# Kernel optimization log

Measured on AMD Instinct MI355X. Metric: run time of the kernel, lower is better.

## Reference

```python
import jax, jax.numpy as jnp
import numpy as np

N, E, R = 10000, 320000, 32
IN, H, OUT, REL_IN = 256, 256, 256, 768
GAMMA = 10.0


def _seg_softmax(logits, seg, n):
    # numerically stable softmax over edges grouped by target node
    m = jax.ops.segment_max(logits, seg, num_segments=n)
    e = jnp.exp(logits - m[seg])
    s = jax.ops.segment_sum(e, seg, num_segments=n)
    return e / (s[seg] + 1e-16)


def _rgat_layer(x, src, dst, etype, W, q, k, n):
    # per-relation linear transform of all nodes: [N, R, H]
    xt = jnp.einsum('ni,rio->nro', x, W)
    xj = xt[src, etype]          # [E, H] transformed source feats
    xi = xt[dst, etype]          # [E, H] transformed target feats
    logits = jax.nn.leaky_relu((xi * q[etype]).sum(-1) + (xj * k[etype]).sum(-1), 0.2)
    a = _seg_softmax(logits, dst, n)            # [E]
    return jax.ops.segment_sum(a[:, None] * xj, dst, num_segments=n)  # [N, H]


def setup_inputs() -> dict:
    key = jax.random.key(0)
    ks = jax.random.split(key, 16)
    s = 0.05
    return {
        'x': jax.random.normal(ks[0], (N, IN), jnp.float32),
        'edge_index': jax.random.randint(ks[1], (2, E), 0, N, jnp.int32),
        'edge_type': jax.random.randint(ks[2], (E,), 0, R, jnp.int32),
        'W1': jax.random.normal(ks[3], (R, IN, H), jnp.float32) * s,
        'q1': jax.random.normal(ks[4], (R, H), jnp.float32) * s,
        'k1': jax.random.normal(ks[5], (R, H), jnp.float32) * s,
        'W2': jax.random.normal(ks[6], (R, H, H), jnp.float32) * s,
        'q2': jax.random.normal(ks[7], (R, H), jnp.float32) * s,
        'k2': jax.random.normal(ks[8], (R, H), jnp.float32) * s,
        'lin_w': jax.random.normal(ks[9], (H, OUT), jnp.float32) * s,
        'lin_b': jnp.zeros((OUT,), jnp.float32),
        'rel_bert': jax.random.normal(ks[10], (R, REL_IN), jnp.float32),
        'rel_lin_w': jax.random.normal(ks[11], (REL_IN, H), jnp.float32) * s,
        'rel_lin_b': jnp.zeros((H,), jnp.float32),
    }


def reference(x, edge_index, edge_type, W1, q1, k1, W2, q2, k2,
              lin_w, lin_b, rel_bert, rel_lin_w, rel_lin_b):
    src, dst = edge_index[0], edge_index[1]
    h = jax.nn.relu(_rgat_layer(x, src, dst, edge_type, W1, q1, k1, N))
    h = jax.nn.relu(_rgat_layer(h, src, dst, edge_type, W2, q2, k2, N))
    h = h @ lin_w + lin_b                                   # [N, OUT]
    # relation embeddings (dropout omitted: eval-mode determinism)
    rel = jax.nn.relu(rel_bert @ rel_lin_w + rel_lin_b)     # [R, H]
    # TransE scoring per edge
    diff = h[src] + rel[edge_type] - h[dst]                 # [E, OUT]
    score = GAMMA - jnp.abs(diff).sum(-1)                   # [E]
    return score
```

## Files before the change

kernel.cpp:

```cpp
#include <hip/hip_runtime.h>
#include <hip/hip_bf16.h>
#include <stdint.h>

#define R_ 32
#define H_ 256
#define GAMMA_ 10.0f

typedef __attribute__((ext_vector_type(4))) float f32x4;
typedef __attribute__((ext_vector_type(8))) short bf16x8;

__device__ __forceinline__ unsigned short f2b(float f){
  union { float f; unsigned u; } v; v.f = f;
  unsigned r = v.u + 0x7FFFu + ((v.u >> 16) & 1u);
  return (unsigned short)(r >> 16);
}
__device__ __forceinline__ float b2f(unsigned short h){
  union { unsigned u; float f; } v; v.u = ((unsigned)h) << 16; return v.f;
}

__global__ __launch_bounds__(256) void prep_kernel(
    const float* __restrict__ x, unsigned short* __restrict__ xb, int n4,
    const float* __restrict__ W1, unsigned short* __restrict__ Wt1,
    const float* __restrict__ W2, unsigned short* __restrict__ Wt2,
    const float* __restrict__ lin_w, unsigned short* __restrict__ linT,
    const float* __restrict__ q1, const float* __restrict__ k1, float* __restrict__ wqkT1,
    const float* __restrict__ q2, const float* __restrict__ k2, float* __restrict__ wqkT2,
    const float* __restrict__ rb, const float* __restrict__ rw,
    const float* __restrict__ rbias, unsigned short* __restrict__ relb,
    const int* __restrict__ dst, const int* __restrict__ et, int* __restrict__ cnt2, int E,
    int nb0, int nb_tw, int nb_lin, int nb_wqk, int nb_rel, int nb_hist){
  __shared__ float tile[32][33];
  const int bx = blockIdx.x, t = threadIdx.x;
  const int b0 = nb0, b1 = b0 + nb_tw, b2 = b1 + nb_tw, b3 = b2 + nb_lin;
  const int b4 = b3 + nb_wqk, b5 = b4 + nb_wqk, b6 = b5 + nb_rel;

  if (bx < b0){
    int i = bx * 256 + t;
    if (i < n4){
      float4 v = ((const float4*)x)[i];
      ushort4 o; o.x=f2b(v.x); o.y=f2b(v.y); o.z=f2b(v.z); o.w=f2b(v.w);
      ((ushort4*)xb)[i] = o;
    }
    return;
  }
  if (bx < b3){
    const float* W; unsigned short* Wt; int local;
    if (bx < b1){ W = W1; Wt = Wt1; local = bx - b0; }
    else if (bx < b2){ W = W2; Wt = Wt2; local = bx - b1; }
    else { W = lin_w; Wt = linT; local = bx - b2; }
    int i0 = (local & 7) * 32, o0 = ((local >> 3) & 7) * 32, r = local >> 6;
    int tx = t & 31, ty = t >> 5;
    const float* Wr = W + (size_t)r * 65536;
    for (int rr = ty; rr < 32; rr += 8)
      tile[rr][tx] = Wr[(size_t)(i0 + rr) * 256 + o0 + tx];
    __syncthreads();
    unsigned short* outr = Wt + (size_t)r * 65536;
    for (int rr = ty; rr < 32; rr += 8)
      outr[(size_t)(o0 + rr) * 256 + i0 + tx] = f2b(tile[tx][rr]);
    return;
  }
  if (bx < b5){
    bool first = bx < b4;
    int local = bx - (first ? b3 : b4);
    int w = t >> 6, lane = t & 63;
    int p = local * 4 + w;
    int i = p & 255, r = p >> 8;
    const float* W  = first ? W1 : W2;
    const float* qv = first ? q1 : q2;
    const float* kv = first ? k1 : k2;
    const float* row = W + ((size_t)r * 256 + i) * 256;
    float sq = 0.f, sk = 0.f;
    #pragma unroll
    for (int q4 = 0; q4 < 4; ++q4){
      int o = lane + q4 * 64;
      float wv = row[o];
      sq += wv * qv[r * 256 + o];
      sk += wv * kv[r * 256 + o];
    }
    #pragma unroll
    for (int o = 32; o; o >>= 1){ sq += __shfl_xor(sq, o); sk += __shfl_xor(sk, o); }
    if (!lane){
      float* wq = first ? wqkT1 : wqkT2;
      wq[i * 64 + r] = sq; wq[i * 64 + 32 + r] = sk;
    }
    return;
  }
  if (bx < b6){
    int r = bx - b5, h = t;
    float acc = rbias[h];
    const float* br = rb + (size_t)r * 768;
    for (int i = 0; i < 768; ++i) acc += br[i] * rw[(size_t)i * 256 + h];
    relb[r * 256 + h] = f2b(fmaxf(acc, 0.f));
    return;
  }
  {
    int e = (bx - b6) * 256 + t;
    if (e < E){
      int d = dst[e];
      atomicAdd(&cnt2[(d >> 5) * 1024 + (d & 31) * 32 + et[e]], 1);
    }
  }
}

__global__ void totred_kernel(const int* __restrict__ cnt2, int* __restrict__ tot){
  __shared__ int red[256];
  int blk = blockIdx.x, t = threadIdx.x;
  int s = 0;
  #pragma unroll
  for (int q = 0; q < 4; ++q) s += cnt2[blk * 1024 + q * 256 + t];
  red[t] = s; __syncthreads();
  for (int o = 128; o; o >>= 1){ if (t < o) red[t] += red[t + o]; __syncthreads(); }
  if (!t) tot[blk] = red[0];
}
__global__ void scan_kernel(const int* __restrict__ deg, int* __restrict__ off, int n){
  __shared__ int carry;
  __shared__ int buf[1024];
  if (threadIdx.x == 0) carry = 0;
  __syncthreads();
  for (int base = 0; base < n; base += 1024){
    int i = base + threadIdx.x;
    int v = (i < n) ? deg[i] : 0;
    buf[threadIdx.x] = v; __syncthreads();
    for (int o = 1; o < 1024; o <<= 1){
      int t = (threadIdx.x >= o) ? buf[threadIdx.x - o] : 0;
      __syncthreads();
      buf[threadIdx.x] += t;
      __syncthreads();
    }
    if (i < n) off[i] = carry + buf[threadIdx.x] - v;
    __syncthreads();
    if (threadIdx.x == 1023) carry += buf[1023];
    __syncthreads();
  }
  if (threadIdx.x == 0) off[n] = carry;
}
__global__ __launch_bounds__(256) void ps2scan_kernel(const int* __restrict__ cnt2, const int* __restrict__ base,
                                                      int* __restrict__ ps2, int nblk, int nbins){
  __shared__ int sb[1024];
  int blk = blockIdx.x, t = threadIdx.x;
  int orig[4];
  #pragma unroll
  for (int q = 0; q < 4; ++q){ int i = q * 256 + t; orig[q] = cnt2[blk * 1024 + i]; sb[i] = orig[q]; }
  __syncthreads();
  for (int o = 1; o < 1024; o <<= 1){
    int v[4];
    #pragma unroll
    for (int q = 0; q < 4; ++q){ int i = q * 256 + t; v[q] = (i >= o) ? sb[i - o] : 0; }
    __syncthreads();
    #pragma unroll
    for (int q = 0; q < 4; ++q){ int i = q * 256 + t; sb[i] += v[q]; }
    __syncthreads();
  }
  int b = base[blk];
  #pragma unroll
  for (int q = 0; q < 4; ++q){ int i = q * 256 + t; ps2[blk * 1024 + i] = b + sb[i] - orig[q]; }
  if (blk == 0 && t == 0) ps2[nbins] = base[nblk];
}
__global__ void scatter2_kernel(const int* __restrict__ src, const int* __restrict__ dst,
                                const int* __restrict__ et, const int* __restrict__ ps2,
                                int* __restrict__ cur2, int* __restrict__ es_src,
                                int* __restrict__ es_et, int E){
  int e = blockIdx.x * 256 + threadIdx.x;
  if (e >= E) return;
  int d = dst[e], r = et[e];
  int key = (d >> 5) * 1024 + (d & 31) * 32 + r;
  int pos = ps2[key] + atomicAdd(&cur2[key], 1);
  es_src[pos] = src[e];
  es_et[pos]  = r;
}

template<int MODE>
__global__ __launch_bounds__(256) void gemmq_kernel(
    const unsigned short* __restrict__ A, const unsigned short* __restrict__ Bt,
    unsigned short* __restrict__ C, const float* __restrict__ bias, int M, int g_gemm,
    const float* __restrict__ wqkT, float* __restrict__ qdot, float* __restrict__ kdot){
  __shared__ unsigned short As[2][128 * 64];
  __shared__ unsigned short Bs[2][128 * 64];
  const int tid = threadIdx.x, lane = tid & 63, wid = tid >> 6;
  const int bx = blockIdx.x;

  if (MODE == 0 && bx >= g_gemm){
    int node = (bx - g_gemm) * 4 + wid;
    if (node >= M) return;
    float* xr = ((float*)As) + wid * 256;
    ushort4 v = ((const ushort4*)(A + (size_t)node * 256))[lane];
    xr[lane * 4 + 0] = b2f(v.x);
    xr[lane * 4 + 1] = b2f(v.y);
    xr[lane * 4 + 2] = b2f(v.z);
    xr[lane * 4 + 3] = b2f(v.w);
    float acc = 0.f;
    #pragma unroll 8
    for (int kk = 0; kk < 256; ++kk)
      acc = fmaf(xr[kk], wqkT[kk * 64 + lane], acc);
    if (lane < 32) qdot[node * 32 + lane] = acc;
    else           kdot[node * 32 + lane - 32] = acc;
    return;
  }

  const int x = (MODE == 0) ? (bx & 63) : (bx & 1);
  const int y = (MODE == 0) ? (bx >> 6) : (bx >> 1);
  const int r = (MODE == 0) ? (x >> 1) : 0;
  const int nbase = (x & 1) * 128;
  const int mbase = y * 128;
  const int wm = (wid >> 1) * 64, wn = (wid & 1) * 64;
  const int lg = lane >> 4, lr = lane & 15;
  const unsigned short* Brel = Bt + (size_t)r * 65536;

  f32x4 acc[4][4];
  #pragma unroll
  for (int i = 0; i < 4; ++i)
    #pragma unroll
    for (int j = 0; j < 4; ++j) acc[i][j] = (f32x4)0.0f;

  auto stage = [&](int buf, int kt){
    #pragma unroll
    for (int q = 0; q < 4; ++q){
      int ci  = (q * 4 + wid) * 64 + lane;
      int row = ci >> 3, p = ci & 7;
      int gch = p ^ (row & 7);
      int grow = mbase + row; if (grow >= M) grow = M - 1;
      const unsigned short* ga = A + (size_t)grow * 256 + kt * 64 + gch * 8;
      __builtin_amdgcn_global_load_lds((const __attribute__((address_space(1))) void*)ga,
          (__attribute__((address_space(3))) void*)(As[buf] + (size_t)(q * 4 + wid) * 512), 16, 0, 0);
      const unsigned short* gb = Brel + (size_t)(nbase + row) * 256 + kt * 64 + gch * 8;
      __builtin_amdgcn_global_load_lds((const __attribute__((address_space(1))) void*)gb,
          (__attribute__((address_space(3))) void*)(Bs[buf] + (size_t)(q * 4 + wid) * 512), 16, 0, 0);
    }
  };

  stage(0, 0);
  __syncthreads();

  for (int kt = 0; kt < 4; ++kt){
    const int cur = kt & 1;
    if (kt < 3) stage(cur ^ 1, kt + 1);
    #pragma unroll
    for (int kk = 0; kk < 2; ++kk){
      bf16x8 af[4], bg[4];
      #pragma unroll
      for (int mi = 0; mi < 4; ++mi){
        int row = wm + mi * 16 + lr;
        int pc = (lg + kk * 4) ^ (row & 7);
        af[mi] = *(const bf16x8*)&As[cur][row * 64 + pc * 8];
      }
      #pragma unroll
      for (int ni = 0; ni < 4; ++ni){
        int row = wn + ni * 16 + lr;
        int pc = (lg + kk * 4) ^ (row & 7);
        bg[ni] = *(const bf16x8*)&Bs[cur][row * 64 + pc * 8];
      }
      #pragma unroll
      for (int mi = 0; mi < 4; ++mi)
        #pragma unroll
        for (int ni = 0; ni < 4; ++ni)
          acc[mi][ni] = __builtin_amdgcn_mfma_f32_16x16x32_bf16(af[mi], bg[ni], acc[mi][ni], 0, 0, 0);
    }
    __syncthreads();
  }

  unsigned short* c_lds = (unsigned short*)As;
  #pragma unroll
  for (int mi = 0; mi < 4; ++mi){
    #pragma unroll
    for (int j = 0; j < 4; ++j){
      int row = wm + mi * 16 + lg * 4 + j;
      #pragma unroll
      for (int ni = 0; ni < 4; ++ni){
        int col = wn + ni * 16 + lr;
        float v = acc[mi][ni][j];
        if (MODE == 1) v += bias[nbase + col];
        c_lds[row * 136 + col] = f2b(v);
      }
    }
  }
  __syncthreads();
  #pragma unroll
  for (int it = 0; it < 8; ++it){
    int c = it * 256 + tid;
    int row = c >> 4, ch = c & 15;
    int rowm = mbase + row;
    if (rowm < M){
      bf16x8 v = *(const bf16x8*)&c_lds[row * 136 + ch * 8];
      if (MODE == 0) *(bf16x8*)&C[((size_t)r * M + rowm) * H_ + nbase + ch * 8] = v;
      else           *(bf16x8*)&C[(size_t)rowm * H_ + nbase + ch * 8] = v;
    }
  }
}

__global__ void attn_agg_kernel(const unsigned short* __restrict__ xt, const float* __restrict__ qdot,
                                const float* __restrict__ kdot, const int* __restrict__ ps2,
                                const int* __restrict__ es_src, const int* __restrict__ es_et,
                                float* __restrict__ a, unsigned short* __restrict__ hout, int n){
  int w = threadIdx.x >> 6, lane = threadIdx.x & 63;
  int node = blockIdx.x * 4 + w;
  if (node >= n) return;
  int kb = (node >> 5) * 1024 + (node & 31) * 32;
  int s = 0, e = 0;
  float qd = 0.f;
  if (lane < 32){
    s = ps2[kb + lane]; e = ps2[kb + lane + 1];
    qd = qdot[node * 32 + lane];
  }
  float m = -1e30f;
  for (int j = s; j < e; ++j){
    float z = qd + kdot[es_src[j] * 32 + lane];
    z = (z > 0.f) ? z : 0.2f * z;
    a[j] = z;
    m = fmaxf(m, z);
  }
  #pragma unroll
  for (int o = 32; o; o >>= 1) m = fmaxf(m, __shfl_xor(m, o));
  float sum = 0.f;
  for (int j = s; j < e; ++j){
    float ez = __expf(a[j] - m);
    a[j] = ez; sum += ez;
  }
  #pragma unroll
  for (int o = 32; o; o >>= 1) sum += __shfl_xor(sum, o);
  float inv = 1.0f / (sum + 1e-16f);
  int s0 = ps2[kb], s1 = ps2[kb + 32];
  float a0 = 0.f, a1 = 0.f, a2 = 0.f, a3 = 0.f;
  int j = s0;
  for (; j + 4 <= s1; j += 4){
    int sc0 = es_src[j],   et0 = es_et[j];
    int sc1 = es_src[j+1], et1 = es_et[j+1];
    int sc2 = es_src[j+2], et2 = es_et[j+2];
    int sc3 = es_src[j+3], et3 = es_et[j+3];
    float w0 = a[j], w1 = a[j+1], w2 = a[j+2], w3 = a[j+3];
    ushort4 v0 = ((const ushort4*)(xt + ((size_t)et0 * n + sc0) * 256))[lane];
    ushort4 v1 = ((const ushort4*)(xt + ((size_t)et1 * n + sc1) * 256))[lane];
    ushort4 v2 = ((const ushort4*)(xt + ((size_t)et2 * n + sc2) * 256))[lane];
    ushort4 v3 = ((const ushort4*)(xt + ((size_t)et3 * n + sc3) * 256))[lane];
    a0 += w0*b2f(v0.x) + w1*b2f(v1.x) + w2*b2f(v2.x) + w3*b2f(v3.x);
    a1 += w0*b2f(v0.y) + w1*b2f(v1.y) + w2*b2f(v2.y) + w3*b2f(v3.y);
    a2 += w0*b2f(v0.z) + w1*b2f(v1.z) + w2*b2f(v2.z) + w3*b2f(v3.z);
    a3 += w0*b2f(v0.w) + w1*b2f(v1.w) + w2*b2f(v2.w) + w3*b2f(v3.w);
  }
  for (; j < s1; ++j){
    int sc = es_src[j], et = es_et[j];
    float wv = a[j];
    ushort4 v = ((const ushort4*)(xt + ((size_t)et * n + sc) * 256))[lane];
    a0 = fmaf(wv, b2f(v.x), a0);
    a1 = fmaf(wv, b2f(v.y), a1);
    a2 = fmaf(wv, b2f(v.z), a2);
    a3 = fmaf(wv, b2f(v.w), a3);
  }
  ushort4 o;
  o.x = f2b(fmaxf(a0 * inv, 0.f)); o.y = f2b(fmaxf(a1 * inv, 0.f));
  o.z = f2b(fmaxf(a2 * inv, 0.f)); o.w = f2b(fmaxf(a3 * inv, 0.f));
  ((ushort4*)(hout + (size_t)node * H_))[lane] = o;
}

__global__ void score_kernel(const unsigned short* __restrict__ hb, const unsigned short* __restrict__ relb,
                             const int* __restrict__ src_a, const int* __restrict__ dst_a,
                             const int* __restrict__ et_a, float* __restrict__ out, int E){
  int e = blockIdx.x * 4 + (threadIdx.x >> 6);
  int lane = threadIdx.x & 63;
  if (e >= E) return;
  int s = src_a[e], d = dst_a[e], r = et_a[e];
  ushort4 a4 = ((const ushort4*)(hb + (size_t)s * H_))[lane];
  ushort4 b4 = ((const ushort4*)(hb + (size_t)d * H_))[lane];
  ushort4 r4 = ((const ushort4*)(relb + (size_t)r * H_))[lane];
  float sum = fabsf(b2f(a4.x) + b2f(r4.x) - b2f(b4.x))
            + fabsf(b2f(a4.y) + b2f(r4.y) - b2f(b4.y))
            + fabsf(b2f(a4.z) + b2f(r4.z) - b2f(b4.z))
            + fabsf(b2f(a4.w) + b2f(r4.w) - b2f(b4.w));
  #pragma unroll
  for (int o = 32; o; o >>= 1) sum += __shfl_xor(sum, o);
  if (!lane) out[e] = GAMMA_ - sum;
}

extern "C" void kernel_launch(void* const* d_in, const int* in_sizes, int n_in,
                              void* d_out, int out_size, void* d_ws, size_t ws_size,
                              hipStream_t stream){
  const float* x         = (const float*)d_in[0];
  const int*   edge_idx  = (const int*)d_in[1];
  const int*   edge_type = (const int*)d_in[2];
  const float* W1        = (const float*)d_in[3];
  const float* q1        = (const float*)d_in[4];
  const float* k1        = (const float*)d_in[5];
  const float* W2        = (const float*)d_in[6];
  const float* q2        = (const float*)d_in[7];
  const float* k2        = (const float*)d_in[8];
  const float* lin_w     = (const float*)d_in[9];
  const float* lin_b     = (const float*)d_in[10];
  const float* rel_bert  = (const float*)d_in[11];
  const float* rel_lin_w = (const float*)d_in[12];
  const float* rel_lin_b = (const float*)d_in[13];
  float* score = (float*)d_out;

  const int Nn = in_sizes[0] / H_;
  const int E  = in_sizes[1] / 2;
  const int* src_a = edge_idx;
  const int* dst_a = edge_idx + E;
  const int NBLK  = (Nn + 31) / 32;
  const int NBINS = NBLK * 1024;

  char* ws = (char*)d_ws;
  size_t cur_off = 0;
  auto carve = [&](size_t bytes)->char*{
    char* p = ws + cur_off;
    cur_off += (bytes + 255) & ~(size_t)255;
    return p;
  };
  unsigned short* xt   = (unsigned short*)carve((size_t)Nn * R_ * H_ * 2);
  unsigned short* xb   = (unsigned short*)carve((size_t)Nn * H_ * 2);
  unsigned short* h1   = (unsigned short*)carve((size_t)Nn * H_ * 2);
  unsigned short* h2   = (unsigned short*)carve((size_t)Nn * H_ * 2);
  unsigned short* outb = (unsigned short*)carve((size_t)Nn * H_ * 2);
  unsigned short* Wt1  = (unsigned short*)carve((size_t)R_ * 65536 * 2);
  unsigned short* Wt2  = (unsigned short*)carve((size_t)R_ * 65536 * 2);
  unsigned short* linT = (unsigned short*)carve(65536 * 2);
  unsigned short* relb = (unsigned short*)carve(R_ * H_ * 2);
  float* wqkT1 = (float*)carve(64 * H_ * 4);
  float* wqkT2 = (float*)carve(64 * H_ * 4);
  float* qdot  = (float*)carve((size_t)Nn * R_ * 4);
  float* kdot  = (float*)carve((size_t)Nn * R_ * 4);
  int* cnt2    = (int*)carve((size_t)NBINS * 4);
  int* cur2    = (int*)carve((size_t)NBINS * 4);
  int* tot     = (int*)carve((size_t)NBLK * 4);
  int* baseA   = (int*)carve((size_t)(NBLK + 1) * 4);
  int* ps2     = (int*)carve((size_t)(NBINS + 1) * 4);
  int* es_src  = (int*)carve((size_t)E * 4);
  int* es_et   = (int*)carve((size_t)E * 4);
  float* attn  = (float*)carve((size_t)E * 4);
  (void)ws_size; (void)n_in; (void)out_size;

  const int mt = (Nn + 127) / 128;
  const int g_gemm = 64 * mt;
  const int nqd = (Nn + 3) / 4;

  const int n4 = Nn * H_ / 4;
  const int nb0 = (n4 + 255) / 256, nb_tw = 2048, nb_lin = 64, nb_wqk = 2048, nb_rel = 32;
  const int nb_hist = (E + 255) / 256;
  const int nprep = nb0 + 2 * nb_tw + nb_lin + 2 * nb_wqk + nb_rel + nb_hist;

  hipMemsetAsync(cnt2, 0, (size_t)NBINS * 4, stream);
  hipMemsetAsync(cur2, 0, (size_t)NBINS * 4, stream);

  prep_kernel<<<nprep, 256, 0, stream>>>(
      x, xb, n4, W1, Wt1, W2, Wt2, lin_w, linT,
      q1, k1, wqkT1, q2, k2, wqkT2,
      rel_bert, rel_lin_w, rel_lin_b, relb,
      dst_a, edge_type, cnt2, E,
      nb0, nb_tw, nb_lin, nb_wqk, nb_rel, nb_hist);

  totred_kernel<<<NBLK, 256, 0, stream>>>(cnt2, tot);
  scan_kernel<<<1, 1024, 0, stream>>>(tot, baseA, NBLK);
  ps2scan_kernel<<<NBLK, 256, 0, stream>>>(cnt2, baseA, ps2, NBLK, NBINS);
  scatter2_kernel<<<(E + 255) / 256, 256, 0, stream>>>(src_a, dst_a, edge_type, ps2, cur2, es_src, es_et, E);

  gemmq_kernel<0><<<g_gemm + nqd, 256, 0, stream>>>(xb, Wt1, xt, nullptr, Nn, g_gemm, wqkT1, qdot, kdot);
  attn_agg_kernel<<<nqd, 256, 0, stream>>>(xt, qdot, kdot, ps2, es_src, es_et, attn, h1, Nn);

  gemmq_kernel<0><<<g_gemm + nqd, 256, 0, stream>>>(h1, Wt2, xt, nullptr, Nn, g_gemm, wqkT2, qdot, kdot);
  attn_agg_kernel<<<nqd, 256, 0, stream>>>(xt, qdot, kdot, ps2, es_src, es_et, attn, h2, Nn);

  gemmq_kernel<1><<<2 * mt, 256, 0, stream>>>(h2, linT, outb, lin_b, Nn, 2 * mt, nullptr, nullptr, nullptr);
  score_kernel<<<(E + 3) / 4, 256, 0, stream>>>(outb, relb, src_a, dst_a, edge_type, score, E);
}
```

Before: 397.8 us.

## Split qdot projection into its own kernel and store GEMM output directly

```diff
diff --git a/kernel.cpp b/kernel.cpp
--- a/kernel.cpp
+++ b/kernel.cpp
@@ -169,39 +169,38 @@
   es_et[pos]  = r;
 }
 
+__global__ void qdot_kernel(const unsigned short* __restrict__ xb, const float* __restrict__ wqkT,
+                            float* __restrict__ qdot, float* __restrict__ kdot, int n){
+  __shared__ float xrow[4][256];
+  int w = threadIdx.x >> 6, lane = threadIdx.x & 63;
+  int node = blockIdx.x * 4 + w;
+  if (node >= n) return;
+  ushort4 v = ((const ushort4*)(xb + (size_t)node * 256))[lane];
+  float* xr = xrow[w];
+  xr[lane * 4 + 0] = b2f(v.x);
+  xr[lane * 4 + 1] = b2f(v.y);
+  xr[lane * 4 + 2] = b2f(v.z);
+  xr[lane * 4 + 3] = b2f(v.w);
+  float acc = 0.f;
+  #pragma unroll 8
+  for (int kk = 0; kk < 256; ++kk)
+    acc = fmaf(xr[kk], wqkT[kk * 64 + lane], acc);
+  if (lane < 32) qdot[node * 32 + lane] = acc;
+  else           kdot[node * 32 + lane - 32] = acc;
+}
+
 template<int MODE>
 __global__ __launch_bounds__(256) void gemmq_kernel(
     const unsigned short* __restrict__ A, const unsigned short* __restrict__ Bt,
-    unsigned short* __restrict__ C, const float* __restrict__ bias, int M, int g_gemm,
-    const float* __restrict__ wqkT, float* __restrict__ qdot, float* __restrict__ kdot){
+    unsigned short* __restrict__ C, const float* __restrict__ bias, int M, int NB){
   __shared__ unsigned short As[2][128 * 64];
   __shared__ unsigned short Bs[2][128 * 64];
-  const int tid = threadIdx.x, lane = tid & 63, wid = tid >> 6;
-  const int bx = blockIdx.x;
-
-  if (MODE == 0 && bx >= g_gemm){
-    int node = (bx - g_gemm) * 4 + wid;
-    if (node >= M) return;
-    float* xr = ((float*)As) + wid * 256;
-    ushort4 v = ((const ushort4*)(A + (size_t)node * 256))[lane];
-    xr[lane * 4 + 0] = b2f(v.x);
-    xr[lane * 4 + 1] = b2f(v.y);
-    xr[lane * 4 + 2] = b2f(v.z);
-    xr[lane * 4 + 3] = b2f(v.w);
-    float acc = 0.f;
-    #pragma unroll 8
-    for (int kk = 0; kk < 256; ++kk)
-      acc = fmaf(xr[kk], wqkT[kk * 64 + lane], acc);
-    if (lane < 32) qdot[node * 32 + lane] = acc;
-    else           kdot[node * 32 + lane - 32] = acc;
-    return;
-  }
-
-  const int x = (MODE == 0) ? (bx & 63) : (bx & 1);
-  const int y = (MODE == 0) ? (bx >> 6) : (bx >> 1);
-  const int r = (MODE == 0) ? (x >> 1) : 0;
-  const int nbase = (x & 1) * 128;
-  const int mbase = y * 128;
+  const int r     = blockIdx.x / NB;
+  const int nbase = (blockIdx.x % NB) * 128;
+  const int mbase = blockIdx.y * 128;
+  const int tid  = threadIdx.x;
+  const int lane = tid & 63;
+  const int wid  = tid >> 6;
   const int wm = (wid >> 1) * 64, wn = (wid & 1) * 64;
   const int lg = lane >> 4, lr = lane & 15;
   const unsigned short* Brel = Bt + (size_t)r * 65536;
@@ -258,31 +257,19 @@
     __syncthreads();
   }
 
-  unsigned short* c_lds = (unsigned short*)As;
   #pragma unroll
   for (int mi = 0; mi < 4; ++mi){
     #pragma unroll
     for (int j = 0; j < 4; ++j){
-      int row = wm + mi * 16 + lg * 4 + j;
+      int rowm = mbase + wm + mi * 16 + lg * 4 + j;
+      if (rowm >= M) continue;
       #pragma unroll
       for (int ni = 0; ni < 4; ++ni){
-        int col = wn + ni * 16 + lr;
+        int col = nbase + wn + ni * 16 + lr;
         float v = acc[mi][ni][j];
-        if (MODE == 1) v += bias[nbase + col];
-        c_lds[row * 136 + col] = f2b(v);
+        if (MODE == 0) C[((size_t)r * M + rowm) * H_ + col] = f2b(v);
+        else           C[(size_t)rowm * H_ + col] = f2b(v + bias[col]);
       }
-    }
-  }
-  __syncthreads();
-  #pragma unroll
-  for (int it = 0; it < 8; ++it){
-    int c = it * 256 + tid;
-    int row = c >> 4, ch = c & 15;
-    int rowm = mbase + row;
-    if (rowm < M){
-      bf16x8 v = *(const bf16x8*)&c_lds[row * 136 + ch * 8];
-      if (MODE == 0) *(bf16x8*)&C[((size_t)r * M + rowm) * H_ + nbase + ch * 8] = v;
-      else           *(bf16x8*)&C[(size_t)rowm * H_ + nbase + ch * 8] = v;
     }
   }
 }
@@ -427,7 +414,6 @@
   (void)ws_size; (void)n_in; (void)out_size;
 
   const int mt = (Nn + 127) / 128;
-  const int g_gemm = 64 * mt;
   const int nqd = (Nn + 3) / 4;
 
   const int n4 = Nn * H_ / 4;
@@ -450,12 +436,14 @@
   ps2scan_kernel<<<NBLK, 256, 0, stream>>>(cnt2, baseA, ps2, NBLK, NBINS);
   scatter2_kernel<<<(E + 255) / 256, 256, 0, stream>>>(src_a, dst_a, edge_type, ps2, cur2, es_src, es_et, E);
 
-  gemmq_kernel<0><<<g_gemm + nqd, 256, 0, stream>>>(xb, Wt1, xt, nullptr, Nn, g_gemm, wqkT1, qdot, kdot);
+  gemmq_kernel<0><<<dim3(R_ * 2, mt), 256, 0, stream>>>(xb, Wt1, xt, nullptr, Nn, 2);
+  qdot_kernel<<<nqd, 256, 0, stream>>>(xb, wqkT1, qdot, kdot, Nn);
   attn_agg_kernel<<<nqd, 256, 0, stream>>>(xt, qdot, kdot, ps2, es_src, es_et, attn, h1, Nn);
 
-  gemmq_kernel<0><<<g_gemm + nqd, 256, 0, stream>>>(h1, Wt2, xt, nullptr, Nn, g_gemm, wqkT2, qdot, kdot);
+  gemmq_kernel<0><<<dim3(R_ * 2, mt), 256, 0, stream>>>(h1, Wt2, xt, nullptr, Nn, 2);
+  qdot_kernel<<<nqd, 256, 0, stream>>>(h1, wqkT2, qdot, kdot, Nn);
   attn_agg_kernel<<<nqd, 256, 0, stream>>>(xt, qdot, kdot, ps2, es_src, es_et, attn, h2, Nn);
 
-  gemmq_kernel<1><<<2 * mt, 256, 0, stream>>>(h2, linT, outb, lin_b, Nn, 2 * mt, nullptr, nullptr, nullptr);
+  gemmq_kernel<1><<<dim3(2, mt), 256, 0, stream>>>(h2, linT, outb, lin_b, Nn, 2);
   score_kernel<<<(E + 3) / 4, 256, 0, stream>>>(outb, relb, src_a, dst_a, edge_type, score, E);
 }
```

After: 416.1 us. +4.6%, slower.
